# Kernel tuning notes

Hardware: AMD Instinct MI355X
Metric: run time of the kernel (lower is better)

Reference implementation:

```python
import jax, jax.numpy as jnp
import numpy as np

B, L = 16384, 200
N_USERS, N_ITEMS, N_CATS, N_DUR = 1_000_000, 100_000, 1000, 50
UD, ID, CD, DD, SD = 64, 64, 16, 8, 64
UDENSE, IDENSE = 25, 3
CONCAT = UD + ID + CD + DD + UDENSE + IDENSE + SD  # 244
NE, EH, EO, NT = 8, 256, 128, 2
T1, T2 = 64, 32  # tower dims
AH1, AH2 = 64, 16  # DIN attention hidden dims
NEG_INF = -1e9


def setup_inputs() -> dict:
    key = jax.random.key(0)
    ks = iter(jax.random.split(key, 40))
    nrm = lambda shape, s: jax.random.normal(next(ks), shape, jnp.float32) * s
    inp = {
        'user_id': jax.random.randint(next(ks), (B,), 0, N_USERS),
        'item_id': jax.random.randint(next(ks), (B,), 0, N_ITEMS),
        'item_category': jax.random.randint(next(ks), (B,), 0, N_CATS),
        'item_dur_bkt': jax.random.randint(next(ks), (B,), 0, N_DUR),
        'user_dense': jax.random.normal(next(ks), (B, UDENSE), jnp.float32),
        'item_dense': jax.random.normal(next(ks), (B, IDENSE), jnp.float32),
        'history_seq': jax.random.randint(next(ks), (B, L), 0, N_ITEMS + 1),
    }
    # embeddings (std=0.01 as in _init_weights); hist row 0 is padding_idx -> zero
    inp['user_E'] = nrm((N_USERS, UD), 0.01)
    inp['item_E'] = nrm((N_ITEMS, ID), 0.01)
    inp['cat_E'] = nrm((N_CATS, CD), 0.01)
    inp['dur_E'] = nrm((N_DUR, DD), 0.01)
    inp['hist_E'] = nrm((N_ITEMS + 1, SD), 0.01).at[0].set(0.0)
    inp['Wproj'] = nrm((ID, SD), 0.12)  # xavier-ish for target_proj (no bias)
    # DIN attention MLP: 4*SD -> 64 -> 16 -> 1
    inp['aW1'] = nrm((4 * SD, AH1), 0.06); inp['ab1'] = jnp.zeros((AH1,), jnp.float32)
    inp['aW2'] = nrm((AH1, AH2), 0.15);    inp['ab2'] = jnp.zeros((AH2,), jnp.float32)
    inp['aW3'] = nrm((AH2, 1), 0.3);       inp['ab3'] = jnp.zeros((1,), jnp.float32)
    # stacked experts: concat -> 256 -> 128 (ReLU both)
    inp['eW1'] = nrm((NE, CONCAT, EH), 0.06); inp['eb1'] = jnp.zeros((NE, EH), jnp.float32)
    inp['eW2'] = nrm((NE, EH, EO), 0.06);     inp['eb2'] = jnp.zeros((NE, EO), jnp.float32)
    # per-task gates: concat -> NE softmax
    inp['gW'] = nrm((NT, CONCAT, NE), 0.06); inp['gb'] = jnp.zeros((NT, NE), jnp.float32)
    # stacked towers: 128 -> 64 -> 32 -> 1
    inp['tW1'] = nrm((NT, EO, T1), 0.09); inp['tb1'] = jnp.zeros((NT, T1), jnp.float32)
    inp['tW2'] = nrm((NT, T1, T2), 0.12); inp['tb2'] = jnp.zeros((NT, T2), jnp.float32)
    inp['tW3'] = nrm((NT, T2, 1), 0.17);  inp['tb3'] = jnp.zeros((NT, 1), jnp.float32)
    return inp


def reference(user_id, item_id, item_category, item_dur_bkt, user_dense, item_dense,
              history_seq, user_E, item_E, cat_E, dur_E, hist_E, Wproj,
              aW1, ab1, aW2, ab2, aW3, ab3,
              eW1, eb1, eW2, eb2, gW, gb,
              tW1, tb1, tW2, tb2, tW3, tb3):
    # --- feature encoding ---
    i_emb = item_E[item_id]            # (B, ID)
    u_emb = user_E[user_id]            # (B, UD)
    c_emb = cat_E[item_category]       # (B, CD)
    d_emb = dur_E[item_dur_bkt]        # (B, DD)
    h_emb = hist_E[history_seq]        # (B, L, SD)
    tgt = (i_emb @ Wproj)[:, None, :]  # (B, 1, SD)
    t = jnp.broadcast_to(tgt, h_emb.shape)
    # DIN attention features: [target, hist, target-hist, target*hist]
    feat = jnp.concatenate([t, h_emb, t - h_emb, t * h_emb], axis=-1)  # (B, L, 4*SD)
    h = jax.nn.relu(feat @ aW1 + ab1)
    h = jax.nn.relu(h @ aW2 + ab2)
    scores = (h @ aW3 + ab3)[..., 0]   # (B, L)
    scores = jnp.where(history_seq == 0, NEG_INF, scores)
    attn = jax.nn.softmax(scores, axis=-1)
    pooled = jnp.einsum('bl,bld->bd', attn, h_emb)  # (B, SD)
    shared = jnp.concatenate([u_emb, i_emb, c_emb, d_emb, user_dense, item_dense, pooled], axis=-1)  # (B, CONCAT)
    # --- experts (batched GEMM) ---
    eh = jax.nn.relu(jnp.einsum('bc,ech->beh', shared, eW1) + eb1)
    eo = jax.nn.relu(jnp.einsum('beh,eho->beo', eh, eW2) + eb2)  # (B, NE, EO)
    # --- per-task gating + towers ---
    gate = jax.nn.softmax(jnp.einsum('bc,tce->bte', shared, gW) + gb, axis=-1)  # (B, T, NE)
    ti = jnp.einsum('bte,beo->bto', gate, eo)  # (B, T, EO)
    x = jax.nn.relu(jnp.einsum('bto,toh->bth', ti, tW1) + tb1)
    x = jax.nn.relu(jnp.einsum('bth,thk->btk', x, tW2) + tb2)
    logit = (jnp.einsum('btk,tkj->btj', x, tW3) + tb3)[..., 0]  # (B, T)
    pred = jax.nn.sigmoid(logit)
    return pred[:, 0], pred[:, 1]
```

## Files before the change

kernel.cpp:

```cpp
#include <hip/hip_runtime.h>
#include <hip/hip_bf16.h>
#include <cstdint>
#include <cmath>


typedef __attribute__((ext_vector_type(8))) short bfrag;
typedef __attribute__((ext_vector_type(4))) float f32x4;

__device__ __forceinline__ unsigned short f2bf(float f) {
  __hip_bfloat16 h = __float2bfloat16(f);
  return __builtin_bit_cast(unsigned short, h);
}
__device__ __forceinline__ float bf2f(unsigned short b) {
  union { unsigned u; float f; } v; v.u = ((unsigned)b) << 16;
  return v.f;
}
__device__ __forceinline__ float bfLo(unsigned hv) {
  union { unsigned u; float f; } v; v.u = hv << 16;
  return v.f;
}
__device__ __forceinline__ float bfHi(unsigned hv) {
  union { unsigned u; float f; } v; v.u = hv & 0xffff0000u;
  return v.f;
}

#define SWZ(row, col) ((col) ^ (((row) & 7) << 3))

static constexpr size_t WS_ATTNB = 0;
static constexpr size_t WS_AW2T  = WS_ATTNB + 16384;
static constexpr size_t WS_A13   = WS_AW2T + 2048;
static constexpr size_t WS_EW1T  = WS_A13 + 16384;
static constexpr size_t WS_EW2T  = WS_EW1T + 1048576;
static constexpr size_t WS_HISTB = WS_EW2T + 524288;
static constexpr size_t WS_TGT   = WS_HISTB + 12800256;
static constexpr size_t WS_TA    = WS_TGT + 2097152;
static constexpr size_t WS_SHP   = WS_TA + 4194304;
static constexpr size_t WS_EO    = WS_SHP + 8388608;
static constexpr size_t WS_GWB   = WS_EO + 33554432;
static constexpr size_t WS_TW1B  = WS_GWB + 8192;
static constexpr size_t WS_TW2B  = WS_TW1B + 32768;
static constexpr size_t WS_WPB   = WS_TW2B + 8192;
static constexpr size_t WS_WAB   = WS_WPB + 8192;

__launch_bounds__(256)
__global__ void k0_prep(const float* __restrict__ aW1, const float* __restrict__ aW2,
                        const float* __restrict__ eW1, const float* __restrict__ eW2,
                        const float* __restrict__ hist_E,
                        const float* __restrict__ gW, const float* __restrict__ tW1,
                        const float* __restrict__ tW2, const float* __restrict__ Wproj,
                        unsigned short* __restrict__ attnBt, unsigned short* __restrict__ aW2t,
                        unsigned short* __restrict__ eW1t, unsigned short* __restrict__ eW2t,
                        unsigned short* __restrict__ hist_b,
                        unsigned short* __restrict__ gWb, unsigned short* __restrict__ tW1b,
                        unsigned short* __restrict__ tW2b,
                        unsigned short* __restrict__ Wpb, unsigned short* __restrict__ WAb) {
  int tid = blockIdx.x * blockDim.x + threadIdx.x;
  int nth = gridDim.x * blockDim.x;
  for (int i = tid; i < 64 * 128; i += nth) {
    int n = i >> 7, k = i & 127;
    float v = (k < 64) ? (aW1[(64 + k) * 64 + n] - aW1[(128 + k) * 64 + n])
                       : aW1[(128 + k) * 64 + n];
    attnBt[i] = f2bf(v);
  }
  for (int i = tid; i < 16 * 64; i += nth) {
    int n = i >> 6, k = i & 63;
    aW2t[i] = f2bf(aW2[k * 16 + n]);
  }
  for (int i = tid; i < 64 * 64; i += nth) {
    int n = i >> 6, k = i & 63;
    Wpb[i] = f2bf(Wproj[k * 64 + n]);
  }
  for (int i = tid; i < 64 * 64; i += nth) {
    int n = i >> 6, k = i & 63;
    float s = 0.f;
    for (int j = 0; j < 64; ++j)
      s += Wproj[k * 64 + j] * (aW1[j * 64 + n] + aW1[(128 + j) * 64 + n]);
    WAb[i] = f2bf(s);
  }
  for (int i = tid; i < 8 * 256 * 256; i += nth) {
    int e = i >> 16, n = (i >> 8) & 255, k = i & 255;
    eW1t[i] = (k < 244) ? f2bf(eW1[(e * 244 + k) * 256 + n]) : (unsigned short)0;
  }
  for (int i = tid; i < 8 * 128 * 256; i += nth) {
    int e = i >> 15, n = (i >> 8) & 127, k = i & 255;
    eW2t[i] = f2bf(eW2[(e * 256 + k) * 128 + n]);
  }
  for (int i = tid; i < 16 * 256; i += nth) {
    int n = i >> 8, k = i & 255, t = n >> 3, e = n & 7;
    gWb[i] = (k < 244) ? f2bf(gW[(t * 244 + k) * 8 + e]) : (unsigned short)0;
  }
  for (int i = tid; i < 2 * 64 * 128; i += nth) {
    int t = i >> 13, n = (i >> 7) & 63, k = i & 127;
    tW1b[i] = f2bf(tW1[(t * 128 + k) * 64 + n]);
  }
  for (int i = tid; i < 2 * 32 * 64; i += nth) {
    int t = i >> 11, n = (i >> 6) & 31, k = i & 63;
    tW2b[i] = f2bf(tW2[(t * 64 + k) * 32 + n]);
  }
  for (int i = tid; i < 100001 * 64; i += nth) hist_b[i] = f2bf(hist_E[i]);
}

__launch_bounds__(256)
__global__ void k1_tgt(const int* __restrict__ item_id, const float* __restrict__ item_E,
                       const unsigned short* __restrict__ Wpb, const unsigned short* __restrict__ WAb,
                       const float* __restrict__ ab1,
                       unsigned short* __restrict__ tgt, float* __restrict__ tA) {
  int tid = threadIdx.x, w = tid >> 6, lane = tid & 63;
  int lr = lane & 15, g = lane >> 4;
  int b0 = blockIdx.x * 64 + w * 16;
  int iid = item_id[b0 + lr];
  bfrag ia[2];
#pragma unroll
  for (int kk = 0; kk < 2; ++kk) {
    const float* src = item_E + (size_t)iid * 64 + kk * 32 + g * 8;
    float4 x = *(const float4*)src;
    float4 y = *(const float4*)(src + 4);
    bfrag r;
    r[0] = (short)f2bf(x.x); r[1] = (short)f2bf(x.y);
    r[2] = (short)f2bf(x.z); r[3] = (short)f2bf(x.w);
    r[4] = (short)f2bf(y.x); r[5] = (short)f2bf(y.y);
    r[6] = (short)f2bf(y.z); r[7] = (short)f2bf(y.w);
    ia[kk] = r;
  }
  f32x4 at[4], aa[4];
#pragma unroll
  for (int i = 0; i < 4; ++i) { at[i] = (f32x4){0,0,0,0}; aa[i] = (f32x4){0,0,0,0}; }
#pragma unroll
  for (int kk = 0; kk < 2; ++kk)
#pragma unroll
    for (int nt = 0; nt < 4; ++nt) {
      bfrag wp = *(const bfrag*)(Wpb + (nt * 16 + lr) * 64 + kk * 32 + g * 8);
      at[nt] = __builtin_amdgcn_mfma_f32_16x16x32_bf16(ia[kk], wp, at[nt], 0, 0, 0);
      bfrag wa = *(const bfrag*)(WAb + (nt * 16 + lr) * 64 + kk * 32 + g * 8);
      aa[nt] = __builtin_amdgcn_mfma_f32_16x16x32_bf16(ia[kk], wa, aa[nt], 0, 0, 0);
    }
#pragma unroll
  for (int nt = 0; nt < 4; ++nt) {
    int n = nt * 16 + lr;
    float b1 = ab1[n];
#pragma unroll
    for (int r = 0; r < 4; ++r) {
      int m = b0 + g * 4 + r;
      tgt[(size_t)m * 64 + n] = f2bf(at[nt][r]);
      tA[(size_t)m * 64 + n] = aa[nt][r] + b1;
    }
  }
}

__launch_bounds__(256, 5)
__global__ void k2_attn(const int* __restrict__ hist_seq, const unsigned short* __restrict__ hist_b,
                        const unsigned short* __restrict__ tgt, const float* __restrict__ tA,
                        const unsigned short* __restrict__ attnBt_g, const unsigned short* __restrict__ aW2t_g,
                        const float* __restrict__ ab2, const float* __restrict__ aW3,
                        const int* __restrict__ user_id, const int* __restrict__ item_id,
                        const int* __restrict__ item_cat, const int* __restrict__ item_dur,
                        const float* __restrict__ user_dense, const float* __restrict__ item_dense,
                        const float* __restrict__ user_E, const float* __restrict__ item_E,
                        const float* __restrict__ cat_E, const float* __restrict__ dur_E,
                        unsigned short* __restrict__ shared_p) {
  __shared__ unsigned short sH1[208 * 64];
  __shared__ int   ids[208];
  __shared__ float tv[64], tAv[64];
  __shared__ float sSc[208];
  __shared__ float red[8];
  __shared__ float pbuf[512];
  int b = blockIdx.x;
  int tid = threadIdx.x, w = tid >> 6, lane = tid & 63;
  int lr = lane & 15, g = lane >> 4;

  if (tid < 208) ids[tid] = (tid < 200) ? hist_seq[(size_t)b * 200 + tid] : 0;
  if (tid < 64) tv[tid] = bf2f(tgt[(size_t)b * 64 + tid]);
  else if (tid < 128) tAv[tid - 64] = tA[(size_t)b * 64 + (tid - 64)];

  {
    unsigned short* row = shared_p + (size_t)b * 256;
    if (tid < 64)       row[tid] = f2bf(user_E[(size_t)user_id[b] * 64 + tid]);
    else if (tid < 128) row[tid] = f2bf(item_E[(size_t)item_id[b] * 64 + (tid - 64)]);
    else if (tid < 144) row[tid] = f2bf(cat_E[item_cat[b] * 16 + (tid - 128)]);
    else if (tid < 152) row[tid] = f2bf(dur_E[item_dur[b] * 8 + (tid - 144)]);
    else if (tid < 177) row[tid] = f2bf(user_dense[b * 25 + (tid - 152)]);
    else if (tid < 180) row[tid] = f2bf(item_dense[b * 3 + (tid - 177)]);
    else if (tid >= 244) row[tid] = 0;
  }

  bfrag b2fr[2];
#pragma unroll
  for (int kk = 0; kk < 2; ++kk)
    b2fr[kk] = *(const bfrag*)(aW2t_g + lr * 64 + kk * 32 + g * 8);
  f32x4 ab2v4 = *(const f32x4*)(ab2 + g * 4);
  f32x4 aW3v4 = *(const f32x4*)(aW3 + g * 4);
  __syncthreads();

  {
    int n = tid >> 2, k0 = (tid & 3) * 16;
    const unsigned short* rowp = attnBt_g + n * 128;
    unsigned short a23[16], a4[16], mo[16];
    *(uint4*)(a23)     = *(const uint4*)(rowp + k0);
    *(uint4*)(a23 + 8) = *(const uint4*)(rowp + k0 + 8);
    *(uint4*)(a4)      = *(const uint4*)(rowp + 64 + k0);
    *(uint4*)(a4 + 8)  = *(const uint4*)(rowp + 64 + k0 + 8);
#pragma unroll
    for (int i = 0; i < 16; ++i)
      mo[i] = f2bf(bf2f(a23[i]) + tv[k0 + i] * bf2f(a4[i]));
    *(uint4*)(sH1 + n * 64 + SWZ(n, k0))     = *(uint4*)(mo);
    *(uint4*)(sH1 + n * 64 + SWZ(n, k0 + 8)) = *(uint4*)(mo + 8);
  }
  __syncthreads();

  bfrag mfr[4][2];
#pragma unroll
  for (int nt = 0; nt < 4; ++nt)
#pragma unroll
    for (int kk = 0; kk < 2; ++kk) {
      int n = nt * 16 + lr;
      mfr[nt][kk] = *(const bfrag*)(sH1 + n * 64 + SWZ(n, kk * 32 + g * 8));
    }
  __syncthreads();

  for (int mt = w; mt < 13; mt += 4) {
    int m = mt * 16 + lr;
    const unsigned short* hrow = hist_b + (size_t)ids[m] * 64;
    bfrag h0 = *(const bfrag*)(hrow + g * 8);
    bfrag h1 = *(const bfrag*)(hrow + 32 + g * 8);
    f32x4 acc[4] = {{0,0,0,0},{0,0,0,0},{0,0,0,0},{0,0,0,0}};
#pragma unroll
    for (int nt = 0; nt < 4; ++nt) {
      acc[nt] = __builtin_amdgcn_mfma_f32_16x16x32_bf16(mfr[nt][0], h0, acc[nt], 0, 0, 0);
      acc[nt] = __builtin_amdgcn_mfma_f32_16x16x32_bf16(mfr[nt][1], h1, acc[nt], 0, 0, 0);
    }
#pragma unroll
    for (int nt = 0; nt < 4; ++nt) {
      f32x4 ta4 = *(const f32x4*)(tAv + nt * 16 + g * 4);
      unsigned lo = (unsigned)f2bf(fmaxf(acc[nt][0] + ta4[0], 0.f))
                  | ((unsigned)f2bf(fmaxf(acc[nt][1] + ta4[1], 0.f)) << 16);
      unsigned hi = (unsigned)f2bf(fmaxf(acc[nt][2] + ta4[2], 0.f))
                  | ((unsigned)f2bf(fmaxf(acc[nt][3] + ta4[3], 0.f)) << 16);
      uint2 pk; pk.x = lo; pk.y = hi;
      *(uint2*)(sH1 + m * 64 + SWZ(m, nt * 16 + g * 4)) = pk;
    }
  }
  __syncthreads();

  for (int mt = w; mt < 13; mt += 4) {
    int m = mt * 16 + lr;
    f32x4 acc2 = {0.f, 0.f, 0.f, 0.f};
#pragma unroll
    for (int kk = 0; kk < 2; ++kk) {
      bfrag hb = *(const bfrag*)(sH1 + m * 64 + SWZ(m, kk * 32 + g * 8));
      acc2 = __builtin_amdgcn_mfma_f32_16x16x32_bf16(b2fr[kk], hb, acc2, 0, 0, 0);
    }
    float p = 0.f;
#pragma unroll
    for (int r = 0; r < 4; ++r)
      p += fmaxf(acc2[r] + ab2v4[r], 0.f) * aW3v4[r];
    p += __shfl_xor(p, 16);
    p += __shfl_xor(p, 32);
    if (lane < 16) sSc[m] = p;
  }
  __syncthreads();

  bool valid = false; float sc0 = 0.f;
  if (tid < 200 && ids[tid] != 0) { valid = true; sc0 = sSc[tid]; }
  float v = valid ? sc0 : -3.0e38f;
#pragma unroll
  for (int d = 1; d < 64; d <<= 1) v = fmaxf(v, __shfl_xor(v, d));
  if (lane == 0) red[w] = v;
  __syncthreads();
  float mx = fmaxf(fmaxf(red[0], red[1]), fmaxf(red[2], red[3]));
  float p = valid ? __expf(sc0 - mx) : 0.f;
  float s = p;
#pragma unroll
  for (int d = 1; d < 64; d <<= 1) s += __shfl_xor(s, d);
  if (lane == 0) red[4 + w] = s;
  if (tid < 208) sSc[tid] = p;
  __syncthreads();
  float denom = red[4] + red[5] + red[6] + red[7] + 1e-30f;

  {
    int hp = lane >> 5, hl = lane & 31;
    float a0 = 0.f, a1 = 0.f;
    for (int i = 0; i < 25; ++i) {
      int l = w * 50 + hp * 25 + i;
      unsigned hv = *(const unsigned*)(hist_b + (size_t)ids[l] * 64 + 2 * hl);
      float pw = sSc[l];
      a0 += pw * bfLo(hv);
      a1 += pw * bfHi(hv);
    }
    pbuf[(w * 2 + hp) * 64 + 2 * hl]     = a0;
    pbuf[(w * 2 + hp) * 64 + 2 * hl + 1] = a1;
  }
  __syncthreads();
  if (tid < 64) {
    float tot = 0.f;
#pragma unroll
    for (int c = 0; c < 8; ++c) tot += pbuf[c * 64 + tid];
    shared_p[(size_t)b * 256 + 180 + tid] = f2bf(tot / denom);
  }
}

__launch_bounds__(256, 2)
__global__ void k3b_experts(const unsigned short* __restrict__ shared_p,
                            const unsigned short* __restrict__ eW1t, const unsigned short* __restrict__ eW2t,
                            const float* __restrict__ eb1, const float* __restrict__ eb2,
                            unsigned short* __restrict__ eo_ws) {
  __shared__ unsigned short sX[64 * 256];
  __shared__ unsigned short sW[256 * 64];
  int tid = threadIdx.x, w = tid >> 6, lane = tid & 63;
  int e = blockIdx.x & 7;
  int b0 = (blockIdx.x >> 3) * 64;
  int lr = lane & 15, g = lane >> 4;

  for (int j = tid; j < 2048; j += 256) {
    int r = j >> 5, ke = (j & 31) * 8;
    uint4 v = *(const uint4*)(shared_p + (size_t)(b0 + r) * 256 + ke);
    *(uint4*)(sX + r * 256 + SWZ(r, ke)) = v;
  }
  f32x4 acc[16];
#pragma unroll
  for (int i = 0; i < 16; ++i) acc[i] = (f32x4){0.f, 0.f, 0.f, 0.f};
  const unsigned short* w1 = eW1t + (size_t)e * 256 * 256;
  for (int c = 0; c < 4; ++c) {
    __syncthreads();
    for (int j = tid; j < 2048; j += 256) {
      int n = j >> 3, ke = (j & 7) * 8;
      uint4 v = *(const uint4*)(w1 + n * 256 + c * 64 + ke);
      *(uint4*)(sW + n * 64 + SWZ(n, ke)) = v;
    }
    __syncthreads();
    int m = w * 16 + lr;
#pragma unroll
    for (int kk = 0; kk < 2; ++kk) {
      int kabs = c * 64 + kk * 32 + g * 8;
      bfrag a = *(const bfrag*)(sX + m * 256 + SWZ(m, kabs));
      int kloc = kk * 32 + g * 8;
#pragma unroll
      for (int nt = 0; nt < 16; ++nt) {
        int n = nt * 16 + lr;
        bfrag bb = *(const bfrag*)(sW + n * 64 + SWZ(n, kloc));
        acc[nt] = __builtin_amdgcn_mfma_f32_16x16x32_bf16(a, bb, acc[nt], 0, 0, 0);
      }
    }
  }
  __syncthreads();
#pragma unroll
  for (int nt = 0; nt < 16; ++nt) {
    int n = nt * 16 + lr;
    float bb = eb1[e * 256 + n];
#pragma unroll
    for (int r = 0; r < 4; ++r) {
      float vv = fmaxf(acc[nt][r] + bb, 0.f);
      int mm = w * 16 + g * 4 + r;
      sX[mm * 256 + SWZ(mm, n)] = f2bf(vv);
    }
  }
  f32x4 acc2[8];
#pragma unroll
  for (int i = 0; i < 8; ++i) acc2[i] = (f32x4){0.f, 0.f, 0.f, 0.f};
  const unsigned short* w2 = eW2t + (size_t)e * 128 * 256;
  for (int c = 0; c < 4; ++c) {
    __syncthreads();
    for (int j = tid; j < 1024; j += 256) {
      int n = j >> 3, ke = (j & 7) * 8;
      uint4 v = *(const uint4*)(w2 + n * 256 + c * 64 + ke);
      *(uint4*)(sW + n * 64 + SWZ(n, ke)) = v;
    }
    __syncthreads();
    int m = w * 16 + lr;
#pragma unroll
    for (int kk = 0; kk < 2; ++kk) {
      int kabs = c * 64 + kk * 32 + g * 8;
      bfrag a = *(const bfrag*)(sX + m * 256 + SWZ(m, kabs));
      int kloc = kk * 32 + g * 8;
#pragma unroll
      for (int nt = 0; nt < 8; ++nt) {
        int n = nt * 16 + lr;
        bfrag bb = *(const bfrag*)(sW + n * 64 + SWZ(n, kloc));
        acc2[nt] = __builtin_amdgcn_mfma_f32_16x16x32_bf16(a, bb, acc2[nt], 0, 0, 0);
      }
    }
  }
#pragma unroll
  for (int nt = 0; nt < 8; ++nt) {
    int n = nt * 16 + lr;
    float bb = eb2[e * 128 + n];
#pragma unroll
    for (int r = 0; r < 4; ++r) {
      float vv = fmaxf(acc2[nt][r] + bb, 0.f);
      int mm = w * 16 + g * 4 + r;
      eo_ws[((size_t)(b0 + mm) * 8 + e) * 128 + n] = f2bf(vv);
    }
  }
}

__launch_bounds__(256, 3)
__global__ void k4_tail(const unsigned short* __restrict__ shared_p, const unsigned short* __restrict__ eo_ws,
                        const unsigned short* __restrict__ gWb, const float* __restrict__ gb,
                        const unsigned short* __restrict__ tW1b, const float* __restrict__ tb1,
                        const unsigned short* __restrict__ tW2b, const float* __restrict__ tb2,
                        const float* __restrict__ tW3, const float* __restrict__ tb3,
                        float* __restrict__ out) {
  __shared__ float sGL[32 * 17];
  __shared__ unsigned short sTi[2 * 32 * 128];
  __shared__ unsigned short sX1[2 * 32 * 64];
  int tid = threadIdx.x, w = tid >> 6, lane = tid & 63;
  int lr = lane & 15, g = lane >> 4;
  int b0 = blockIdx.x * 32;

  if (w < 2) {
    int m = b0 + w * 16 + lr;
    f32x4 acc = {0.f, 0.f, 0.f, 0.f};
#pragma unroll
    for (int kk = 0; kk < 8; ++kk) {
      bfrag a = *(const bfrag*)(shared_p + (size_t)m * 256 + kk * 32 + g * 8);
      bfrag bb = *(const bfrag*)(gWb + lr * 256 + kk * 32 + g * 8);
      acc = __builtin_amdgcn_mfma_f32_16x16x32_bf16(a, bb, acc, 0, 0, 0);
    }
    float gbv = gb[lr];
#pragma unroll
    for (int r = 0; r < 4; ++r)
      sGL[(w * 16 + g * 4 + r) * 17 + lr] = acc[r] + gbv;
  }
  __syncthreads();

  if (tid < 64) {
    int row = tid >> 1, t = tid & 1;
    float* p = sGL + row * 17 + t * 8;
    float mx = -3e38f;
#pragma unroll
    for (int e = 0; e < 8; ++e) mx = fmaxf(mx, p[e]);
    float sum = 0.f; float pe[8];
#pragma unroll
    for (int e = 0; e < 8; ++e) { pe[e] = __expf(p[e] - mx); sum += pe[e]; }
    float inv = 1.f / sum;
#pragma unroll
    for (int e = 0; e < 8; ++e) p[e] = pe[e] * inv;
  }
  __syncthreads();

  {
    int row = tid >> 3, q = tid & 7, t = q >> 2, o0 = (q & 3) * 32;
    const float* gp = sGL + row * 17 + t * 8;
    float accL[16], accH[16];
#pragma unroll
    for (int j = 0; j < 16; ++j) { accL[j] = 0.f; accH[j] = 0.f; }
    const unsigned short* base = eo_ws + ((size_t)(b0 + row) * 8) * 128 + o0;
#pragma unroll
    for (int e = 0; e < 8; ++e) {
      float ge = gp[e];
      const unsigned short* p = base + e * 128;
#pragma unroll
      for (int c = 0; c < 4; ++c) {
        uint4 v = *(const uint4*)(p + c * 8);
        const unsigned* u = (const unsigned*)&v;
#pragma unroll
        for (int j = 0; j < 4; ++j) {
          accL[c * 4 + j] += ge * bfLo(u[j]);
          accH[c * 4 + j] += ge * bfHi(u[j]);
        }
      }
    }
    unsigned short ob[32];
#pragma unroll
    for (int j = 0; j < 16; ++j) {
      ob[2 * j]     = f2bf(accL[j]);
      ob[2 * j + 1] = f2bf(accH[j]);
    }
#pragma unroll
    for (int c = 0; c < 4; ++c)
      *(uint4*)(sTi + t * 4096 + row * 128 + SWZ(row, o0 + c * 8)) = *(const uint4*)(ob + c * 8);
  }
  __syncthreads();

  int t = w >> 1, mt = w & 1;
  {
    f32x4 acc[4] = {{0.f,0.f,0.f,0.f},{0.f,0.f,0.f,0.f},{0.f,0.f,0.f,0.f},{0.f,0.f,0.f,0.f}};
    int ml = mt * 16 + lr;
#pragma unroll
    for (int kk = 0; kk < 4; ++kk) {
      bfrag a = *(const bfrag*)(sTi + t * 4096 + ml * 128 + SWZ(ml, kk * 32 + g * 8));
#pragma unroll
      for (int nt = 0; nt < 4; ++nt) {
        bfrag bb = *(const bfrag*)(tW1b + t * 8192 + (nt * 16 + lr) * 128 + kk * 32 + g * 8);
        acc[nt] = __builtin_amdgcn_mfma_f32_16x16x32_bf16(a, bb, acc[nt], 0, 0, 0);
      }
    }
#pragma unroll
    for (int nt = 0; nt < 4; ++nt) {
      int n = nt * 16 + lr;
      float bias = tb1[t * 64 + n];
#pragma unroll
      for (int r = 0; r < 4; ++r) {
        float x = fmaxf(acc[nt][r] + bias, 0.f);
        int row = mt * 16 + g * 4 + r;
        sX1[t * 2048 + row * 64 + SWZ(row, n)] = f2bf(x);
      }
    }
  }
  __syncthreads();

  {
    f32x4 acc[2] = {{0.f,0.f,0.f,0.f},{0.f,0.f,0.f,0.f}};
    int ml = mt * 16 + lr;
#pragma unroll
    for (int kk = 0; kk < 2; ++kk) {
      bfrag a = *(const bfrag*)(sX1 + t * 2048 + ml * 64 + SWZ(ml, kk * 32 + g * 8));
#pragma unroll
      for (int nt = 0; nt < 2; ++nt) {
        bfrag bb = *(const bfrag*)(tW2b + t * 2048 + (nt * 16 + lr) * 64 + kk * 32 + g * 8);
        acc[nt] = __builtin_amdgcn_mfma_f32_16x16x32_bf16(a, bb, acc[nt], 0, 0, 0);
      }
    }
    float part[4] = {0.f, 0.f, 0.f, 0.f};
#pragma unroll
    for (int nt = 0; nt < 2; ++nt) {
      int n = nt * 16 + lr;
      float bias = tb2[t * 32 + n];
      float w3 = tW3[t * 32 + n];
#pragma unroll
      for (int r = 0; r < 4; ++r)
        part[r] += fmaxf(acc[nt][r] + bias, 0.f) * w3;
    }
#pragma unroll
    for (int d = 1; d < 16; d <<= 1)
#pragma unroll
      for (int r = 0; r < 4; ++r) part[r] += __shfl_xor(part[r], d);
    if (lr == 0) {
      float b3 = tb3[t];
#pragma unroll
      for (int r = 0; r < 4; ++r) {
        float logit = part[r] + b3;
        out[(size_t)t * 16384 + b0 + mt * 16 + g * 4 + r] = 1.f / (1.f + __expf(-logit));
      }
    }
  }
}

extern "C" void kernel_launch(void* const* d_in, const int* in_sizes, int n_in,
                              void* d_out, int out_size, void* d_ws, size_t ws_size,
                              hipStream_t stream) {
  const int*   user_id    = (const int*)  d_in[0];
  const int*   item_id    = (const int*)  d_in[1];
  const int*   item_cat   = (const int*)  d_in[2];
  const int*   item_dur   = (const int*)  d_in[3];
  const float* user_dense = (const float*)d_in[4];
  const float* item_dense = (const float*)d_in[5];
  const int*   hist_seq   = (const int*)  d_in[6];
  const float* user_E     = (const float*)d_in[7];
  const float* item_E     = (const float*)d_in[8];
  const float* cat_E      = (const float*)d_in[9];
  const float* dur_E      = (const float*)d_in[10];
  const float* hist_E     = (const float*)d_in[11];
  const float* Wproj      = (const float*)d_in[12];
  const float* aW1        = (const float*)d_in[13];
  const float* ab1        = (const float*)d_in[14];
  const float* aW2        = (const float*)d_in[15];
  const float* ab2        = (const float*)d_in[16];
  const float* aW3        = (const float*)d_in[17];
  const float* eW1        = (const float*)d_in[19];
  const float* eb1        = (const float*)d_in[20];
  const float* eW2        = (const float*)d_in[21];
  const float* eb2        = (const float*)d_in[22];
  const float* gW         = (const float*)d_in[23];
  const float* gb         = (const float*)d_in[24];
  const float* tW1        = (const float*)d_in[25];
  const float* tb1        = (const float*)d_in[26];
  const float* tW2        = (const float*)d_in[27];
  const float* tb2        = (const float*)d_in[28];
  const float* tW3        = (const float*)d_in[29];
  const float* tb3        = (const float*)d_in[30];
  float* out = (float*)d_out;
  char* ws = (char*)d_ws;

  unsigned short* attnBt  = (unsigned short*)(ws + WS_ATTNB);
  unsigned short* aW2t    = (unsigned short*)(ws + WS_AW2T);
  unsigned short* eW1t    = (unsigned short*)(ws + WS_EW1T);
  unsigned short* eW2t    = (unsigned short*)(ws + WS_EW2T);
  unsigned short* hist_b  = (unsigned short*)(ws + WS_HISTB);
  unsigned short* tgt     = (unsigned short*)(ws + WS_TGT);
  float*          tA      = (float*)         (ws + WS_TA);
  unsigned short* shared_p= (unsigned short*)(ws + WS_SHP);
  unsigned short* eo_ws   = (unsigned short*)(ws + WS_EO);
  unsigned short* gWb     = (unsigned short*)(ws + WS_GWB);
  unsigned short* tW1b    = (unsigned short*)(ws + WS_TW1B);
  unsigned short* tW2b    = (unsigned short*)(ws + WS_TW2B);
  unsigned short* Wpb     = (unsigned short*)(ws + WS_WPB);
  unsigned short* WAb     = (unsigned short*)(ws + WS_WAB);

  k0_prep<<<2048, 256, 0, stream>>>(aW1, aW2, eW1, eW2, hist_E, gW, tW1, tW2, Wproj,
                                    attnBt, aW2t, eW1t, eW2t, hist_b,
                                    gWb, tW1b, tW2b, Wpb, WAb);
  k1_tgt<<<256, 256, 0, stream>>>(item_id, item_E, Wpb, WAb, ab1, tgt, tA);
  k2_attn<<<16384, 256, 0, stream>>>(hist_seq, hist_b, tgt, tA, attnBt, aW2t,
                                     ab2, aW3,
                                     user_id, item_id, item_cat, item_dur,
                                     user_dense, item_dense, user_E, item_E,
                                     cat_E, dur_E, shared_p);
  k3b_experts<<<2048, 256, 0, stream>>>(shared_p, eW1t, eW2t, eb1, eb2, eo_ws);
  k4_tail<<<512, 256, 0, stream>>>(shared_p, eo_ws, gWb, gb, tW1b, tb1, tW2b, tb2,
                                   tW3, tb3, out);
}
```

Measured before the change: 257.3 us.

## Split shared-row assembly into own kernel and halve attention LDS buffer for occupancy

The gather of user, item, category and duration embeddings plus dense features into the shared row moves out of the attention kernel into a separate light kernel, so the attention kernel does less work per block. Inside the attention kernel, the first-layer activation buffer in LDS is cut from 208 to 112 rows by running the two attention MLP layers in two halves over the history. Launch bounds rise from 5 to 8 blocks per CU to make use of the smaller LDS footprint. The cost is one extra kernel launch, two more block barriers, and tighter register limits that could cause spilling.

```diff
diff --git a/kernel.cpp b/kernel.cpp
--- a/kernel.cpp
+++ b/kernel.cpp
@@ -147,18 +147,32 @@
   }
 }
 
-__launch_bounds__(256, 5)
+__launch_bounds__(256)
+__global__ void k3a_assemble(const int* __restrict__ user_id, const int* __restrict__ item_id,
+                             const int* __restrict__ item_cat, const int* __restrict__ item_dur,
+                             const float* __restrict__ user_dense, const float* __restrict__ item_dense,
+                             const float* __restrict__ user_E, const float* __restrict__ item_E,
+                             const float* __restrict__ cat_E, const float* __restrict__ dur_E,
+                             unsigned short* __restrict__ shared_p) {
+  int tid = threadIdx.x, w = tid >> 6, lane = tid & 63;
+  int b = blockIdx.x * 4 + w;
+  unsigned short* row = shared_p + (size_t)b * 256;
+  row[lane]      = f2bf(user_E[(size_t)user_id[b] * 64 + lane]);
+  row[64 + lane] = f2bf(item_E[(size_t)item_id[b] * 64 + lane]);
+  if (lane < 16) row[128 + lane] = f2bf(cat_E[item_cat[b] * 16 + lane]);
+  if (lane < 8)  row[144 + lane] = f2bf(dur_E[item_dur[b] * 8 + lane]);
+  if (lane < 25) row[152 + lane] = f2bf(user_dense[b * 25 + lane]);
+  if (lane < 3)  row[177 + lane] = f2bf(item_dense[b * 3 + lane]);
+  if (lane < 12) row[244 + lane] = 0;
+}
+
+__launch_bounds__(256, 8)
 __global__ void k2_attn(const int* __restrict__ hist_seq, const unsigned short* __restrict__ hist_b,
                         const unsigned short* __restrict__ tgt, const float* __restrict__ tA,
                         const unsigned short* __restrict__ attnBt_g, const unsigned short* __restrict__ aW2t_g,
                         const float* __restrict__ ab2, const float* __restrict__ aW3,
-                        const int* __restrict__ user_id, const int* __restrict__ item_id,
-                        const int* __restrict__ item_cat, const int* __restrict__ item_dur,
-                        const float* __restrict__ user_dense, const float* __restrict__ item_dense,
-                        const float* __restrict__ user_E, const float* __restrict__ item_E,
-                        const float* __restrict__ cat_E, const float* __restrict__ dur_E,
                         unsigned short* __restrict__ shared_p) {
-  __shared__ unsigned short sH1[208 * 64];
+  __shared__ unsigned short sH1[112 * 64];
   __shared__ int   ids[208];
   __shared__ float tv[64], tAv[64];
   __shared__ float sSc[208];
@@ -172,17 +186,6 @@
   if (tid < 64) tv[tid] = bf2f(tgt[(size_t)b * 64 + tid]);
   else if (tid < 128) tAv[tid - 64] = tA[(size_t)b * 64 + (tid - 64)];
 
-  {
-    unsigned short* row = shared_p + (size_t)b * 256;
-    if (tid < 64)       row[tid] = f2bf(user_E[(size_t)user_id[b] * 64 + tid]);
-    else if (tid < 128) row[tid] = f2bf(item_E[(size_t)item_id[b] * 64 + (tid - 64)]);
-    else if (tid < 144) row[tid] = f2bf(cat_E[item_cat[b] * 16 + (tid - 128)]);
-    else if (tid < 152) row[tid] = f2bf(dur_E[item_dur[b] * 8 + (tid - 144)]);
-    else if (tid < 177) row[tid] = f2bf(user_dense[b * 25 + (tid - 152)]);
-    else if (tid < 180) row[tid] = f2bf(item_dense[b * 3 + (tid - 177)]);
-    else if (tid >= 244) row[tid] = 0;
-  }
-
   bfrag b2fr[2];
 #pragma unroll
   for (int kk = 0; kk < 2; ++kk)
@@ -217,47 +220,54 @@
     }
   __syncthreads();
 
-  for (int mt = w; mt < 13; mt += 4) {
-    int m = mt * 16 + lr;
-    const unsigned short* hrow = hist_b + (size_t)ids[m] * 64;
-    bfrag h0 = *(const bfrag*)(hrow + g * 8);
-    bfrag h1 = *(const bfrag*)(hrow + 32 + g * 8);
-    f32x4 acc[4] = {{0,0,0,0},{0,0,0,0},{0,0,0,0},{0,0,0,0}};
-#pragma unroll
-    for (int nt = 0; nt < 4; ++nt) {
-      acc[nt] = __builtin_amdgcn_mfma_f32_16x16x32_bf16(mfr[nt][0], h0, acc[nt], 0, 0, 0);
-      acc[nt] = __builtin_amdgcn_mfma_f32_16x16x32_bf16(mfr[nt][1], h1, acc[nt], 0, 0, 0);
-    }
-#pragma unroll
-    for (int nt = 0; nt < 4; ++nt) {
-      f32x4 ta4 = *(const f32x4*)(tAv + nt * 16 + g * 4);
-      unsigned lo = (unsigned)f2bf(fmaxf(acc[nt][0] + ta4[0], 0.f))
-                  | ((unsigned)f2bf(fmaxf(acc[nt][1] + ta4[1], 0.f)) << 16);
-      unsigned hi = (unsigned)f2bf(fmaxf(acc[nt][2] + ta4[2], 0.f))
-                  | ((unsigned)f2bf(fmaxf(acc[nt][3] + ta4[3], 0.f)) << 16);
-      uint2 pk; pk.x = lo; pk.y = hi;
-      *(uint2*)(sH1 + m * 64 + SWZ(m, nt * 16 + g * 4)) = pk;
-    }
-  }
-  __syncthreads();
-
-  for (int mt = w; mt < 13; mt += 4) {
-    int m = mt * 16 + lr;
-    f32x4 acc2 = {0.f, 0.f, 0.f, 0.f};
-#pragma unroll
-    for (int kk = 0; kk < 2; ++kk) {
-      bfrag hb = *(const bfrag*)(sH1 + m * 64 + SWZ(m, kk * 32 + g * 8));
-      acc2 = __builtin_amdgcn_mfma_f32_16x16x32_bf16(b2fr[kk], hb, acc2, 0, 0, 0);
-    }
-    float p = 0.f;
-#pragma unroll
-    for (int r = 0; r < 4; ++r)
-      p += fmaxf(acc2[r] + ab2v4[r], 0.f) * aW3v4[r];
-    p += __shfl_xor(p, 16);
-    p += __shfl_xor(p, 32);
-    if (lane < 16) sSc[m] = p;
-  }
-  __syncthreads();
+#pragma unroll
+  for (int half = 0; half < 2; ++half) {
+    int tlo = half ? 7 : 0;
+    int thi = half ? 13 : 7;
+    int base = half * 112;
+    for (int mt = tlo + w; mt < thi; mt += 4) {
+      int m = mt * 16 + lr;
+      int mloc = m - base;
+      const unsigned short* hrow = hist_b + (size_t)ids[m] * 64;
+      bfrag h0 = *(const bfrag*)(hrow + g * 8);
+      bfrag h1 = *(const bfrag*)(hrow + 32 + g * 8);
+      f32x4 acc[4] = {{0,0,0,0},{0,0,0,0},{0,0,0,0},{0,0,0,0}};
+#pragma unroll
+      for (int nt = 0; nt < 4; ++nt) {
+        acc[nt] = __builtin_amdgcn_mfma_f32_16x16x32_bf16(mfr[nt][0], h0, acc[nt], 0, 0, 0);
+        acc[nt] = __builtin_amdgcn_mfma_f32_16x16x32_bf16(mfr[nt][1], h1, acc[nt], 0, 0, 0);
+      }
+#pragma unroll
+      for (int nt = 0; nt < 4; ++nt) {
+        f32x4 ta4 = *(const f32x4*)(tAv + nt * 16 + g * 4);
+        unsigned lo = (unsigned)f2bf(fmaxf(acc[nt][0] + ta4[0], 0.f))
+                    | ((unsigned)f2bf(fmaxf(acc[nt][1] + ta4[1], 0.f)) << 16);
+        unsigned hi = (unsigned)f2bf(fmaxf(acc[nt][2] + ta4[2], 0.f))
+                    | ((unsigned)f2bf(fmaxf(acc[nt][3] + ta4[3], 0.f)) << 16);
+        uint2 pk; pk.x = lo; pk.y = hi;
+        *(uint2*)(sH1 + mloc * 64 + SWZ(mloc, nt * 16 + g * 4)) = pk;
+      }
+    }
+    __syncthreads();
+    for (int mt = tlo + w; mt < thi; mt += 4) {
+      int m = mt * 16 + lr;
+      int mloc = m - base;
+      f32x4 acc2 = {0.f, 0.f, 0.f, 0.f};
+#pragma unroll
+      for (int kk = 0; kk < 2; ++kk) {
+        bfrag hb = *(const bfrag*)(sH1 + mloc * 64 + SWZ(mloc, kk * 32 + g * 8));
+        acc2 = __builtin_amdgcn_mfma_f32_16x16x32_bf16(b2fr[kk], hb, acc2, 0, 0, 0);
+      }
+      float p = 0.f;
+#pragma unroll
+      for (int r = 0; r < 4; ++r)
+        p += fmaxf(acc2[r] + ab2v4[r], 0.f) * aW3v4[r];
+      p += __shfl_xor(p, 16);
+      p += __shfl_xor(p, 32);
+      if (lane < 16) sSc[m] = p;
+    }
+    __syncthreads();
+  }
 
   bool valid = false; float sc0 = 0.f;
   if (tid < 200 && ids[tid] != 0) { valid = true; sc0 = sSc[tid]; }
@@ -590,11 +600,11 @@
                                     attnBt, aW2t, eW1t, eW2t, hist_b,
                                     gWb, tW1b, tW2b, Wpb, WAb);
   k1_tgt<<<256, 256, 0, stream>>>(item_id, item_E, Wpb, WAb, ab1, tgt, tA);
+  k3a_assemble<<<4096, 256, 0, stream>>>(user_id, item_id, item_cat, item_dur,
+                                         user_dense, item_dense, user_E, item_E,
+                                         cat_E, dur_E, shared_p);
   k2_attn<<<16384, 256, 0, stream>>>(hist_seq, hist_b, tgt, tA, attnBt, aW2t,
-                                     ab2, aW3,
-                                     user_id, item_id, item_cat, item_dur,
-                                     user_dense, item_dense, user_E, item_E,
-                                     cat_E, dur_E, shared_p);
+                                     ab2, aW3, shared_p);
   k3b_experts<<<2048, 256, 0, stream>>>(shared_p, eW1t, eW2t, eb1, eb2, eo_ws);
   k4_tail<<<512, 256, 0, stream>>>(shared_p, eo_ws, gWb, gb, tW1b, tb1, tW2b, tb2,
                                    tW3, tb3, out);
```

Result: slower. 701.0 us (+172.4%).
